# Optimization experiments

Measured on AMD Instinct MI355X. Metric: run time of the kernel, lower is better.

The kernel has to match this reference:

```python
import jax, jax.numpy as jnp
import numpy as np

B, T, C, H = 4, 2048, 1024, 16
D = C // H  # head_dim = 64


def setup_inputs() -> dict:
    key = jax.random.key(0)
    ks = jax.random.split(key, 5)
    scale = 0.02
    return {
        "x": jax.random.normal(ks[0], (B, T, C), dtype=jnp.float32),
        "w_qkv": jax.random.normal(ks[1], (C, 3 * C), dtype=jnp.float32) * scale,
        "b_qkv": jnp.zeros((3 * C,), dtype=jnp.float32),
        "w_out": jax.random.normal(ks[2], (C, C), dtype=jnp.float32) * scale,
        "b_out": jnp.zeros((C,), dtype=jnp.float32),
    }


def reference(x, w_qkv, b_qkv, w_out, b_out):
    Bx, Tx, Cx = x.shape
    qkv = x @ w_qkv + b_qkv  # [B,T,3C]
    q, k, v = jnp.split(qkv, 3, axis=-1)
    # [B,T,C] -> [B,H,T,D]
    def heads(t):
        return t.reshape(Bx, Tx, H, D).transpose(0, 2, 1, 3)
    q, k, v = heads(q), heads(k), heads(v)
    scores = jnp.einsum("bhtd,bhsd->bhts", q, k) / jnp.sqrt(jnp.float32(D))
    causal = jnp.tril(jnp.ones((Tx, Tx), dtype=bool))
    scores = jnp.where(causal[None, None], scores, -jnp.inf)
    attn = jax.nn.softmax(scores, axis=-1)
    y = jnp.einsum("bhts,bhsd->bhtd", attn, v)  # [B,H,T,D]
    y = y.transpose(0, 2, 1, 3).reshape(Bx, Tx, Cx)
    return y @ w_out + b_out
```

## Files before the change

### kernel.cpp

```cpp
#include <hip/hip_runtime.h>
#include <hip/hip_bf16.h>
#include <math.h>

typedef __bf16 bf16;
typedef __bf16 bf16x8 __attribute__((ext_vector_type(8)));
typedef __bf16 bf16x4 __attribute__((ext_vector_type(4)));
typedef float  f32x4  __attribute__((ext_vector_type(4)));

__device__ __forceinline__ void gld_lds16(const bf16* g, bf16* l) {
    void* gv = (void*)g;
    __builtin_amdgcn_global_load_lds(
        (__attribute__((address_space(1))) void*)gv,
        (__attribute__((address_space(3))) void*)l, 16, 0, 0);
}

__global__ void k_cvt_bf16(const float* __restrict__ in, bf16* __restrict__ out, int n4) {
    int i = blockIdx.x * blockDim.x + threadIdx.x;
    if (i < n4) {
        float4 v = ((const float4*)in)[i];
        bf16x4 o;
        o[0] = (bf16)v.x; o[1] = (bf16)v.y; o[2] = (bf16)v.z; o[3] = (bf16)v.w;
        ((bf16x4*)out)[i] = o;
    }
}

__global__ void k_transpose_cvt(const float* __restrict__ in, bf16* __restrict__ out,
                                int R, int C) {
    __shared__ float tile[64][68];
    int c0 = blockIdx.x * 64, r0 = blockIdx.y * 64;
    int tid = threadIdx.x;
#pragma unroll
    for (int i = 0; i < 4; ++i) {
        int chunk = tid + i * 256;
        int r = chunk >> 4, c4 = (chunk & 15) * 4;
        float4 v = *(const float4*)(in + (size_t)(r0 + r) * C + c0 + c4);
        tile[r][c4 + 0] = v.x; tile[r][c4 + 1] = v.y;
        tile[r][c4 + 2] = v.z; tile[r][c4 + 3] = v.w;
    }
    __syncthreads();
#pragma unroll
    for (int i = 0; i < 2; ++i) {
        int chunk = tid + i * 256;
        int c = chunk >> 3, k8 = (chunk & 7) * 8;
        bf16x8 v;
#pragma unroll
        for (int j = 0; j < 8; ++j) v[j] = (bf16)tile[k8 + j][c];
        *(bf16x8*)(out + (size_t)(c0 + c) * R + r0 + k8) = v;
    }
}

__global__ void k_transpose_v(const bf16* __restrict__ qkv, bf16* __restrict__ vt) {
    __shared__ bf16 tile[64][72];
    int bh = blockIdx.y, b = bh >> 4, h = bh & 15;
    int t0 = blockIdx.x * 64;
    int tid = threadIdx.x;
    const bf16* src = qkv + (size_t)(b * 2048 + t0) * 3072 + 2048 + h * 64;
#pragma unroll
    for (int i = 0; i < 2; ++i) {
        int chunk = tid + i * 256;
        int t = chunk >> 3, d8 = (chunk & 7) * 8;
        bf16x8 v = *(const bf16x8*)(src + (size_t)t * 3072 + d8);
#pragma unroll
        for (int j = 0; j < 8; ++j) tile[t][d8 + j] = v[j];
    }
    __syncthreads();
#pragma unroll
    for (int i = 0; i < 2; ++i) {
        int chunk = tid + i * 256;
        int d = chunk >> 3, t8 = (chunk & 7) * 8;
        bf16x8 v;
#pragma unroll
        for (int j = 0; j < 8; ++j) v[j] = tile[t8 + j][d];
        *(bf16x8*)(vt + ((size_t)bh * 64 + d) * 2048 + t0 + t8) = v;
    }
}

template <bool OUT_BF16>
__global__ __launch_bounds__(256, 2) void k_gemm(
    const bf16* __restrict__ A, const bf16* __restrict__ Bt,
    const float* __restrict__ bias, void* __restrict__ Cout,
    int M, int N, int K) {
    __shared__ __align__(16) bf16 lA[2][4096];
    __shared__ __align__(16) bf16 lB[2][4096];
    int tid = threadIdx.x;
    int wid = tid >> 6, lane = tid & 63;
    int quad = lane >> 4, l16 = lane & 15;
    int bm = blockIdx.y * 128, bn = blockIdx.x * 128;
    int wm = (wid >> 1) * 64, wn = (wid & 1) * 64;

    f32x4 zero = {0.f, 0.f, 0.f, 0.f};
    f32x4 acc[4][4];
#pragma unroll
    for (int i = 0; i < 4; ++i)
#pragma unroll
        for (int j = 0; j < 4; ++j) acc[i][j] = zero;

    for (int k0 = 0; k0 < K; k0 += 64) {
        __syncthreads();
#pragma unroll
        for (int i = 0; i < 4; ++i) {
            int j = (wid * 4 + i) * 64 + lane;
            int kf = j >> 9, row = (j & 511) >> 2, c8 = (j & 3) * 8;
            gld_lds16(A  + (size_t)(bm + row) * K + k0 + kf * 32 + c8, &lA[0][0] + (wid * 4 + i) * 512);
            gld_lds16(Bt + (size_t)(bn + row) * K + k0 + kf * 32 + c8, &lB[0][0] + (wid * 4 + i) * 512);
        }
        __syncthreads();
#pragma unroll
        for (int kk = 0; kk < 2; ++kk) {
            bf16x8 af[4], bg[4];
#pragma unroll
            for (int i = 0; i < 4; ++i) {
                af[i] = *(const bf16x8*)(&lA[kk][(wm + i * 16 + l16) * 32 + quad * 8]);
                bg[i] = *(const bf16x8*)(&lB[kk][(wn + i * 16 + l16) * 32 + quad * 8]);
            }
#pragma unroll
            for (int i = 0; i < 4; ++i)
#pragma unroll
                for (int j = 0; j < 4; ++j)
                    acc[i][j] = __builtin_amdgcn_mfma_f32_16x16x32_bf16(af[i], bg[j], acc[i][j], 0, 0, 0);
        }
    }
#pragma unroll
    for (int i = 0; i < 4; ++i) {
#pragma unroll
        for (int j = 0; j < 4; ++j) {
            int col = bn + wn + j * 16 + l16;
            float bv = bias ? bias[col] : 0.f;
#pragma unroll
            for (int r = 0; r < 4; ++r) {
                int row = bm + wm + i * 16 + quad * 4 + r;
                float v = acc[i][j][r] + bv;
                if (OUT_BF16) ((bf16*)Cout)[(size_t)row * N + col] = (bf16)v;
                else          ((float*)Cout)[(size_t)row * N + col] = v;
            }
        }
    }
}

__global__ __launch_bounds__(256, 3) void k_attn(
    const bf16* __restrict__ qkv,
    const bf16* __restrict__ vt,
    bf16* __restrict__ y) {
    __shared__ __align__(16) bf16 lK[2][4096];
    __shared__ __align__(16) bf16 lV[2][4096];
    __shared__ __align__(16) bf16 lP[4][32 * 72];

    const int T = 2048, CQ = 3072;
    int tid = threadIdx.x, wid = tid >> 6, lane = tid & 63;
    int quad = lane >> 4, l16 = lane & 15;
    int x = blockIdx.x;
    int bh = ((x & 7) << 3) | ((x >> 3) & 7);
    int qb = 15 - (x >> 6);
    int b = bh >> 4, h = bh & 15;
    int q0 = qb * 128;
    int rb = qb * 4 + wid;
    int mdiag = rb >> 1;
    int ntiles = qb * 2 + 2;

    const bf16* qbase = qkv + (size_t)(b * T + q0 + wid * 32) * CQ + h * 64;
    const bf16* kbase = qkv + (size_t)(b * T) * CQ + 1024 + h * 64;
    const bf16* vbase = vt + (size_t)bh * 64 * T;
    bf16* lPw = lP[wid];

    auto stage = [&](int kt, int buf) {
        int t0 = kt * 64;
#pragma unroll
        for (int i = 0; i < 2; ++i) {
            int j = (wid * 2 + i) * 64 + lane;
            int kf = j >> 8, r = (j & 255) >> 2, c8 = (j & 3) * 8;
            gld_lds16(kbase + (size_t)(t0 + r) * CQ + kf * 32 + c8, &lK[buf][(wid * 2 + i) * 512]);
            gld_lds16(vbase + (size_t)r * T + t0 + kf * 32 + c8,    &lV[buf][(wid * 2 + i) * 512]);
        }
    };

    bf16x8 qf[2][2];
#pragma unroll
    for (int qi = 0; qi < 2; ++qi)
#pragma unroll
        for (int kf = 0; kf < 2; ++kf) {
            bf16x8 v = *(const bf16x8*)(qbase + (size_t)(qi * 16 + l16) * CQ + kf * 32 + quad * 8);
#pragma unroll
            for (int j = 0; j < 8; ++j) v[j] = (bf16)((float)v[j] * 0.125f);
            qf[qi][kf] = v;
        }

    f32x4 zero = {0.f, 0.f, 0.f, 0.f};
    f32x4 m10 = {-10.f, -10.f, -10.f, -10.f};
    f32x4 o[2][4];
    float lsum[2] = {0.f, 0.f};
#pragma unroll
    for (int qi = 0; qi < 2; ++qi)
#pragma unroll
        for (int i = 0; i < 4; ++i) o[qi][i] = zero;

    stage(0, 0);
    for (int kt = 0; kt < ntiles; ++kt) {
        __syncthreads();
        if (kt + 1 < ntiles) stage(kt + 1, (kt + 1) & 1);
        if (kt > mdiag) continue;
        const bf16* Kb = lK[kt & 1];
        const bf16* Vb = lV[kt & 1];
        bool diag = (kt == mdiag);
        bool half = diag && !(rb & 1);
        int in_hi = half ? 2 : 4;

        f32x4 s[2][4];
#pragma unroll
        for (int qi = 0; qi < 2; ++qi)
#pragma unroll
            for (int in = 0; in < 4; ++in) s[qi][in] = m10;
        for (int kf = 0; kf < 2; ++kf)
            for (int in = 0; in < in_hi; ++in) {
                bf16x8 kb = *(const bf16x8*)(Kb + kf * 2048 + (in * 16 + l16) * 32 + quad * 8);
#pragma unroll
                for (int qi = 0; qi < 2; ++qi)
                    s[qi][in] = __builtin_amdgcn_mfma_f32_16x16x32_bf16(kb, qf[qi][kf], s[qi][in], 0, 0, 0);
            }

        bf16x8 vb[2][4];
#pragma unroll
        for (int kf = 0; kf < 2; ++kf)
#pragma unroll
            for (int dn = 0; dn < 4; ++dn)
                vb[kf][dn] = *(const bf16x8*)(Vb + kf * 2048 + (dn * 16 + l16) * 32 + quad * 8);

        int rl0 = (rb * 32) - kt * 64;
        for (int qi = 0; qi < 2; ++qi) {
            int qloc = rl0 + qi * 16 + l16;
#pragma unroll
            for (int in = 0; in < 4; ++in) {
                bf16x4 pk4;
                if (in >= in_hi) {
                    pk4[0] = pk4[1] = pk4[2] = pk4[3] = (bf16)0.f;
                } else {
#pragma unroll
                    for (int r = 0; r < 4; ++r) {
                        float e = __expf(s[qi][in][r]);
                        if (diag) {
                            int tloc = in * 16 + quad * 4 + r;
                            if (tloc > qloc) e = 0.f;
                        }
                        lsum[qi] += e;
                        pk4[r] = (bf16)e;
                    }
                }
                *(bf16x4*)(lPw + (qi * 16 + l16) * 72 + in * 16 + quad * 4) = pk4;
            }
        }

#pragma unroll
        for (int qi = 0; qi < 2; ++qi)
#pragma unroll
            for (int kf = 0; kf < 2; ++kf) {
                bf16x8 pa = *(const bf16x8*)(lPw + (qi * 16 + l16) * 72 + kf * 32 + quad * 8);
#pragma unroll
                for (int dn = 0; dn < 4; ++dn)
                    o[qi][dn] = __builtin_amdgcn_mfma_f32_16x16x32_bf16(pa, vb[kf][dn], o[qi][dn], 0, 0, 0);
            }
    }

    float linv[2];
#pragma unroll
    for (int qi = 0; qi < 2; ++qi) {
        float l = lsum[qi];
        l += __shfl_xor(l, 16, 64);
        l += __shfl_xor(l, 32, 64);
        linv[qi] = 1.f / l;
    }
#pragma unroll
    for (int qi = 0; qi < 2; ++qi)
#pragma unroll
        for (int r = 0; r < 4; ++r) {
            float li = __shfl(linv[qi], quad * 4 + r, 64);
            int row = q0 + wid * 32 + qi * 16 + quad * 4 + r;
#pragma unroll
            for (int dn = 0; dn < 4; ++dn) {
                float v = o[qi][dn][r] * li;
                y[(size_t)(b * T + row) * 1024 + h * 64 + dn * 16 + l16] = (bf16)v;
            }
        }
}

extern "C" void kernel_launch(void* const* d_in, const int* in_sizes, int n_in,
                              void* d_out, int out_size, void* d_ws, size_t ws_size,
                              hipStream_t stream) {
    const float* x     = (const float*)d_in[0];
    const float* w_qkv = (const float*)d_in[1];
    const float* b_qkv = (const float*)d_in[2];
    const float* w_out = (const float*)d_in[3];
    const float* b_out = (const float*)d_in[4];
    float* out = (float*)d_out;

    const int B = 4, T = 2048, C = 1024, H = 16;
    const int M = B * T;

    char* ws = (char*)d_ws;
    bf16* xb    = (bf16*)(ws);
    bf16* wqkvT = (bf16*)(ws + (16ull << 20));
    bf16* woutT = (bf16*)(ws + (22ull << 20));
    bf16* qkvb  = (bf16*)(ws + (24ull << 20));
    bf16* yb    = (bf16*)(ws + (72ull << 20));
    bf16* vtb   = xb;

    k_cvt_bf16<<<(M * C / 4 + 255) / 256, 256, 0, stream>>>(x, xb, M * C / 4);
    k_transpose_cvt<<<dim3(3 * C / 64, C / 64), 256, 0, stream>>>(w_qkv, wqkvT, C, 3 * C);
    k_transpose_cvt<<<dim3(C / 64, C / 64), 256, 0, stream>>>(w_out, woutT, C, C);
    k_gemm<true><<<dim3(3 * C / 128, M / 128), 256, 0, stream>>>(xb, wqkvT, b_qkv, qkvb, M, 3 * C, C);
    k_transpose_v<<<dim3(T / 64, B * H), 256, 0, stream>>>(qkvb, vtb);
    k_attn<<<dim3(1024, 1), 256, 0, stream>>>(qkvb, vtb, yb);
    k_gemm<false><<<dim3(C / 128, M / 128), 256, 0, stream>>>(yb, woutT, b_out, out, M, C, C);
}
```

Measured before the change: 274.4 us.

## Swizzle K/V LDS layout, use exp2 with folded log2e, compute row sums via MFMA

Replaces the split-kf K/V LDS tile layout with a 64-wide row layout whose 16-byte chunks are XOR-swizzled by row, so the MFMA operand reads avoid LDS bank conflicts. Folds log2(e) into the Q pre-scale and the fixed max offset so the softmax can use the hardware exp2 instead of expf. Row sums now come from an extra MFMA against a ones vector using the bf16-rounded probabilities, replacing per-element scalar accumulation and the final shuffle reduction. This adds one MFMA per P fragment.

```diff
diff --git a/kernel.cpp b/kernel.cpp
--- a/kernel.cpp
+++ b/kernel.cpp
@@ -5,6 +5,7 @@
 typedef __bf16 bf16;
 typedef __bf16 bf16x8 __attribute__((ext_vector_type(8)));
 typedef __bf16 bf16x4 __attribute__((ext_vector_type(4)));
+typedef __bf16 bf16x2 __attribute__((ext_vector_type(2)));
 typedef float  f32x4  __attribute__((ext_vector_type(4)));
 
 __device__ __forceinline__ void gld_lds16(const bf16* g, bf16* l) {
@@ -167,12 +168,14 @@
 #pragma unroll
         for (int i = 0; i < 2; ++i) {
             int j = (wid * 2 + i) * 64 + lane;
-            int kf = j >> 8, r = (j & 255) >> 2, c8 = (j & 3) * 8;
-            gld_lds16(kbase + (size_t)(t0 + r) * CQ + kf * 32 + c8, &lK[buf][(wid * 2 + i) * 512]);
-            gld_lds16(vbase + (size_t)r * T + t0 + kf * 32 + c8,    &lV[buf][(wid * 2 + i) * 512]);
+            int r = j >> 3;
+            int cs = ((j ^ r) & 7) * 8;
+            gld_lds16(kbase + (size_t)(t0 + r) * CQ + cs, &lK[buf][(wid * 2 + i) * 512]);
+            gld_lds16(vbase + (size_t)r * T + t0 + cs,    &lV[buf][(wid * 2 + i) * 512]);
         }
     };
 
+    const float QSCALE = 0.125f * 1.44269504088896341f;
     bf16x8 qf[2][2];
 #pragma unroll
     for (int qi = 0; qi < 2; ++qi)
@@ -180,18 +183,23 @@
         for (int kf = 0; kf < 2; ++kf) {
             bf16x8 v = *(const bf16x8*)(qbase + (size_t)(qi * 16 + l16) * CQ + kf * 32 + quad * 8);
 #pragma unroll
-            for (int j = 0; j < 8; ++j) v[j] = (bf16)((float)v[j] * 0.125f);
+            for (int j = 0; j < 8; ++j) v[j] = (bf16)((float)v[j] * QSCALE);
             qf[qi][kf] = v;
         }
 
     f32x4 zero = {0.f, 0.f, 0.f, 0.f};
-    f32x4 m10 = {-10.f, -10.f, -10.f, -10.f};
+    f32x4 minit = {-14.4269504089f, -14.4269504089f, -14.4269504089f, -14.4269504089f};
     f32x4 o[2][4];
-    float lsum[2] = {0.f, 0.f};
-#pragma unroll
-    for (int qi = 0; qi < 2; ++qi)
+    f32x4 ls[2];
+#pragma unroll
+    for (int qi = 0; qi < 2; ++qi) {
+        ls[qi] = zero;
 #pragma unroll
         for (int i = 0; i < 4; ++i) o[qi][i] = zero;
+    }
+    bf16x8 ones;
+#pragma unroll
+    for (int j = 0; j < 8; ++j) ones[j] = (bf16)1.0f;
 
     stage(0, 0);
     for (int kt = 0; kt < ntiles; ++kt) {
@@ -208,10 +216,11 @@
 #pragma unroll
         for (int qi = 0; qi < 2; ++qi)
 #pragma unroll
-            for (int in = 0; in < 4; ++in) s[qi][in] = m10;
+            for (int in = 0; in < 4; ++in) s[qi][in] = minit;
+#pragma unroll
         for (int kf = 0; kf < 2; ++kf)
             for (int in = 0; in < in_hi; ++in) {
-                bf16x8 kb = *(const bf16x8*)(Kb + kf * 2048 + (in * 16 + l16) * 32 + quad * 8);
+                bf16x8 kb = *(const bf16x8*)(Kb + (in * 16 + l16) * 64 + (((kf * 4 + quad) ^ (l16 & 7)) * 8));
 #pragma unroll
                 for (int qi = 0; qi < 2; ++qi)
                     s[qi][in] = __builtin_amdgcn_mfma_f32_16x16x32_bf16(kb, qf[qi][kf], s[qi][in], 0, 0, 0);
@@ -222,7 +231,7 @@
         for (int kf = 0; kf < 2; ++kf)
 #pragma unroll
             for (int dn = 0; dn < 4; ++dn)
-                vb[kf][dn] = *(const bf16x8*)(Vb + kf * 2048 + (dn * 16 + l16) * 32 + quad * 8);
+                vb[kf][dn] = *(const bf16x8*)(Vb + (dn * 16 + l16) * 64 + (((kf * 4 + quad) ^ (l16 & 7)) * 8));
 
         int rl0 = (rb * 32) - kt * 64;
         for (int qi = 0; qi < 2; ++qi) {
@@ -235,12 +244,11 @@
                 } else {
 #pragma unroll
                     for (int r = 0; r < 4; ++r) {
-                        float e = __expf(s[qi][in][r]);
+                        float e = __builtin_amdgcn_exp2f(s[qi][in][r]);
                         if (diag) {
                             int tloc = in * 16 + quad * 4 + r;
                             if (tloc > qloc) e = 0.f;
                         }
-                        lsum[qi] += e;
                         pk4[r] = (bf16)e;
                     }
                 }
@@ -253,25 +261,18 @@
 #pragma unroll
             for (int kf = 0; kf < 2; ++kf) {
                 bf16x8 pa = *(const bf16x8*)(lPw + (qi * 16 + l16) * 72 + kf * 32 + quad * 8);
+                ls[qi] = __builtin_amdgcn_mfma_f32_16x16x32_bf16(pa, ones, ls[qi], 0, 0, 0);
 #pragma unroll
                 for (int dn = 0; dn < 4; ++dn)
                     o[qi][dn] = __builtin_amdgcn_mfma_f32_16x16x32_bf16(pa, vb[kf][dn], o[qi][dn], 0, 0, 0);
             }
     }
 
-    float linv[2];
-#pragma unroll
-    for (int qi = 0; qi < 2; ++qi) {
-        float l = lsum[qi];
-        l += __shfl_xor(l, 16, 64);
-        l += __shfl_xor(l, 32, 64);
-        linv[qi] = 1.f / l;
-    }
 #pragma unroll
     for (int qi = 0; qi < 2; ++qi)
 #pragma unroll
         for (int r = 0; r < 4; ++r) {
-            float li = __shfl(linv[qi], quad * 4 + r, 64);
+            float li = 1.f / ls[qi][r];
             int row = q0 + wid * 32 + qi * 16 + quad * 4 + r;
 #pragma unroll
             for (int dn = 0; dn < 4; ++dn) {
```

New measurement: 288.7 us. 1.05x slower.
